# Performance work log

Hardware: AMD Instinct MI355X
Metric: run time of the kernel (lower is better)

## Reference

```python
import jax, jax.numpy as jnp
import numpy as np

D_MODEL = 2048
N_HEADS = 16
HEAD_DIM = D_MODEL // N_HEADS  # 128
MAX_POS = 2048


def _precompute_cos_sin(max_pos, head_dim):
    inv_freq = 1.0 / (10000.0 ** (jnp.arange(0, head_dim, 2, dtype=jnp.float32) / head_dim))
    t = jnp.arange(max_pos, dtype=jnp.float32)
    freqs = jnp.outer(t, inv_freq)          # [max_pos, head_dim//2]
    emb = jnp.concatenate([freqs, freqs], axis=-1)  # [max_pos, head_dim]
    return jnp.cos(emb), jnp.sin(emb)


def _rotate_half(x):
    x1, x2 = x[..., : x.shape[-1] // 2], x[..., x.shape[-1] // 2 :]
    return jnp.concatenate([-x2, x1], axis=-1)


def setup_inputs() -> dict:
    key = jax.random.key(0)
    kx, kq, kk, kv, ko = jax.random.split(key, 5)
    B, S = 2, 2048
    x = jax.random.normal(kx, (B, S, D_MODEL), dtype=jnp.float32)
    scale = 1.0 / np.sqrt(D_MODEL)
    # torch Linear weights are [out_features, in_features]
    Wq = jax.random.normal(kq, (D_MODEL, D_MODEL), dtype=jnp.float32) * scale
    Wk = jax.random.normal(kk, (D_MODEL, D_MODEL), dtype=jnp.float32) * scale
    Wv = jax.random.normal(kv, (D_MODEL, D_MODEL), dtype=jnp.float32) * scale
    Wo = jax.random.normal(ko, (D_MODEL, D_MODEL), dtype=jnp.float32) * scale
    cos, sin = _precompute_cos_sin(MAX_POS, HEAD_DIM)
    # causal mask: True where attention is disallowed (masked_fill semantics)
    mask = jnp.triu(jnp.ones((S, S), dtype=bool), k=1)
    mask = jnp.broadcast_to(mask[None], (B, S, S))
    return {"x": x, "Wq": Wq, "Wk": Wk, "Wv": Wv, "Wo": Wo,
            "cos": cos, "sin": sin, "mask": mask}


def reference(x, Wq, Wk, Wv, Wo, cos, sin, mask):
    B, S, _ = x.shape
    H, Dh = N_HEADS, HEAD_DIM
    scaling = Dh ** -0.5

    def split_heads(y):  # [B,S,D] -> [B,H,S,Dh]
        return y.reshape(B, S, H, Dh).transpose(0, 2, 1, 3)

    q = split_heads(x @ Wq.T)
    k = split_heads(x @ Wk.T)
    v = split_heads(x @ Wv.T)

    c = cos[:S][None, None]  # [1,1,S,Dh]
    s = sin[:S][None, None]
    q = q * c + _rotate_half(q) * s
    k = k * c + _rotate_half(k) * s

    scores = jnp.einsum("bhqd,bhkd->bhqk", q, k) * scaling
    scores = jnp.where(mask[:, None], -jnp.inf, scores)
    attn = jax.nn.softmax(scores, axis=-1)
    out = jnp.einsum("bhqk,bhkd->bhqd", attn, v)  # [B,H,S,Dh]
    out = out.transpose(0, 2, 1, 3).reshape(B, S, H * Dh)
    return out @ Wo.T
```

## Files before the change

kernel.cpp:

```cpp
#include <hip/hip_runtime.h>

typedef float f32x4 __attribute__((ext_vector_type(4)));
typedef short s16x8 __attribute__((ext_vector_type(8)));
typedef unsigned short u16;
typedef u16 u16x4 __attribute__((ext_vector_type(4)));

#define SEQ 2048
#define BATCH 2
#define NH 16
#define DH 128
#define DM 2048
#define MROWS (BATCH * SEQ)

__device__ constexpr float SCALE2 = 0.12751879523531f;

__device__ __forceinline__ u16 f2bf(float f) {
  unsigned u = __float_as_uint(f);
  u += 0x7fffu + ((u >> 16) & 1u);
  return (u16)(u >> 16);
}
__device__ __forceinline__ float bf2f(u16 b) {
  return __uint_as_float(((unsigned)b) << 16);
}

__device__ __forceinline__ void gld_lds16(const void* g, void* l) {
  __builtin_amdgcn_global_load_lds(
      (const __attribute__((address_space(1))) unsigned int*)g,
      (__attribute__((address_space(3))) unsigned int*)l, 16, 0, 0);
}

__global__ __launch_bounds__(256) void cast_all(const float* __restrict__ x,
                                                const float* __restrict__ Wq,
                                                const float* __restrict__ Wk,
                                                const float* __restrict__ Wv,
                                                const float* __restrict__ Wo,
                                                u16* __restrict__ xb,
                                                u16* __restrict__ Wqkvb,
                                                u16* __restrict__ Wob) {
  long i = (long)blockIdx.x * 256 + threadIdx.x;
  const float* src;
  u16* dst;
  long off;
  if (i < 2097152)      { src = x;  dst = xb;              off = i; }
  else if (i < 3145728) { src = Wq; dst = Wqkvb;           off = i - 2097152; }
  else if (i < 4194304) { src = Wk; dst = Wqkvb + 4194304; off = i - 3145728; }
  else if (i < 5242880) { src = Wv; dst = Wqkvb + 8388608; off = i - 4194304; }
  else                  { src = Wo; dst = Wob;             off = i - 5242880; }
  float4 v = ((const float4*)src)[off];
  u16x4 o;
  o[0] = f2bf(v.x); o[1] = f2bf(v.y); o[2] = f2bf(v.z); o[3] = f2bf(v.w);
  ((u16x4*)dst)[off] = o;
}

template <bool F32OUT>
__global__ __launch_bounds__(256) void gemm_bt(const u16* __restrict__ A,
                                               const u16* __restrict__ B,
                                               void* __restrict__ Cv,
                                               int M, int N, int K) {
  __shared__ u16 As[128 * 32];
  __shared__ u16 Bs[128 * 32];
  const int tid = threadIdx.x;
  const int wave = tid >> 6;
  const int lane = tid & 63;
  const int r = lane & 15, g = lane >> 4;

  const int mtiles = M >> 7;
  const int nwg = mtiles * (N >> 7);
  const int cpx = nwg >> 3;
  const int bid = blockIdx.x;
  const int swz = (bid & 7) * cpx + (bid >> 3);
  const int m0 = (swz % mtiles) * 128;
  const int n0 = (swz / mtiles) * 128;

  const int wm = (wave >> 1) * 64;
  const int wn = (wave & 1) * 64;

  f32x4 acc[4][4] = {};

  const int row0 = tid >> 2;
  const int col0 = (tid & 3) * 8;
  const u16* ga0 = A + (long)(m0 + row0) * K + col0;
  const u16* ga1 = A + (long)(m0 + 64 + row0) * K + col0;
  const u16* gb0 = B + (long)(n0 + row0) * K + col0;
  const u16* gb1 = B + (long)(n0 + 64 + row0) * K + col0;

  u16* lA0 = &As[wave * 512];
  u16* lA1 = &As[2048 + wave * 512];
  u16* lB0 = &Bs[wave * 512];
  u16* lB1 = &Bs[2048 + wave * 512];

  for (int k0 = 0; k0 < K; k0 += 32) {
    gld_lds16(ga0 + k0, lA0);
    gld_lds16(ga1 + k0, lA1);
    gld_lds16(gb0 + k0, lB0);
    gld_lds16(gb1 + k0, lB1);
    __syncthreads();
    s16x8 af[4], bfr[4];
#pragma unroll
    for (int i = 0; i < 4; i++) {
      af[i]  = *(const s16x8*)&As[(wm + i * 16 + r) * 32 + g * 8];
      bfr[i] = *(const s16x8*)&Bs[(wn + i * 16 + r) * 32 + g * 8];
    }
#pragma unroll
    for (int i = 0; i < 4; i++)
#pragma unroll
      for (int j = 0; j < 4; j++)
        acc[i][j] = __builtin_amdgcn_mfma_f32_16x16x32_bf16(af[i], bfr[j], acc[i][j], 0, 0, 0);
    __syncthreads();
  }

  float* Cf = (float*)Cv;
  u16* Cb = (u16*)Cv;
#pragma unroll
  for (int i = 0; i < 4; i++)
#pragma unroll
    for (int j = 0; j < 4; j++) {
      const int row = m0 + wm + i * 16 + g * 4;
      const int col = n0 + wn + j * 16 + r;
#pragma unroll
      for (int q = 0; q < 4; q++) {
        float v = acc[i][j][q];
        if (F32OUT) Cf[(long)(row + q) * N + col] = v;
        else        Cb[(long)(row + q) * N + col] = f2bf(v);
      }
    }
}

__global__ __launch_bounds__(512, 2) void gemm_qkv8(const u16* __restrict__ A,
                                                    const u16* __restrict__ B,
                                                    u16* __restrict__ Qo,
                                                    u16* __restrict__ Ko,
                                                    u16* __restrict__ Vo) {
  __shared__ u16 Alds[2][256 * 64];
  __shared__ u16 Blds[2][128 * 64];
  const int tid = threadIdx.x, wave = tid >> 6, lane = tid & 63;
  const int r = lane & 15, g = lane >> 4;
  const int wm = wave >> 1, wn = wave & 1;
  const int bid = blockIdx.x;
  const int swz = (bid & 7) * 96 + (bid >> 3);
  const int m0 = (swz & 15) * 256;
  const int n0 = (swz >> 4) * 128;

  const int lrow = lane >> 3;
  const int csrc = (lane & 7) ^ lrow;

  f32x4 acc[4][4] = {};
  s16x8 aF[2][4], bF[2][4];

#define STAGE_A(TA, MH, BUF) do {                                             \
  _Pragma("unroll") for (int i_ = 0; i_ < 2; ++i_) {                          \
    const int row0_ = (MH) * 128 + i_ * 64 + wave * 8;                        \
    gld_lds16(A + (long)(m0 + row0_ + lrow) * 2048 + (TA) * 64 + csrc * 8,    \
              &Alds[BUF][row0_ * 64]);                                        \
  } } while (0)
#define STAGE_B(TA, NHh, BUF) do {                                            \
    const int row0_ = (NHh) * 64 + wave * 8;                                  \
    gld_lds16(B + (long)(n0 + row0_ + lrow) * 2048 + (TA) * 64 + csrc * 8,    \
              &Blds[BUF][row0_ * 64]);                                        \
  } while (0)

#define READ_K(KK) do {                                                       \
  _Pragma("unroll") for (int mf = 0; mf < 4; ++mf) {                          \
    const int arow = wm * 64 + mf * 16 + r;                                   \
    aF[KK][mf] = *(const s16x8*)&Ab[arow * 64 +                               \
                                    ((((KK) * 4 + g) ^ (arow & 7)) * 8)];     \
  }                                                                           \
  _Pragma("unroll") for (int nf = 0; nf < 4; ++nf) {                          \
    const int brow = wn * 64 + nf * 16 + r;                                   \
    bF[KK][nf] = *(const s16x8*)&Bb[brow * 64 +                               \
                                    ((((KK) * 4 + g) ^ (brow & 7)) * 8)];     \
  } } while (0)

#define MFMA_K(KK) do {                                                       \
  __builtin_amdgcn_s_setprio(1);                                              \
  _Pragma("unroll") for (int mf = 0; mf < 4; ++mf)                            \
    _Pragma("unroll") for (int nf = 0; nf < 4; ++nf)                          \
      acc[mf][nf] = __builtin_amdgcn_mfma_f32_16x16x32_bf16(                  \
          aF[KK][mf], bF[KK][nf], acc[mf][nf], 0, 0, 0);                      \
  __builtin_amdgcn_s_setprio(0);                                              \
} while (0)

  STAGE_A(0, 0, 0); STAGE_B(0, 0, 0); STAGE_A(0, 1, 0); STAGE_B(0, 1, 0);
  STAGE_A(1, 0, 1); STAGE_B(1, 0, 1);
  asm volatile("s_waitcnt vmcnt(3)" ::: "memory");
  __builtin_amdgcn_s_barrier();

  for (int t = 0; t < 32; ++t) {
    const int bt = t & 1, bn = bt ^ 1;
    const u16* Ab = Alds[bt];
    const u16* Bb = Blds[bt];

    READ_K(0);
    __builtin_amdgcn_sched_barrier(0);
    READ_K(1);
    if (t < 31) { STAGE_A(t + 1, 1, bn); STAGE_B(t + 1, 1, bn); }

    asm volatile("s_waitcnt lgkmcnt(8)" ::: "memory");
    __builtin_amdgcn_sched_barrier(0);
    MFMA_K(0);

    asm volatile("s_waitcnt lgkmcnt(0)" ::: "memory");
    __builtin_amdgcn_sched_barrier(0);
    __builtin_amdgcn_s_barrier();

    if (t < 30) { STAGE_A(t + 2, 0, bt); STAGE_B(t + 2, 0, bt); }
    MFMA_K(1);

    if (t < 30)       asm volatile("s_waitcnt vmcnt(3)" ::: "memory");
    else if (t == 30) asm volatile("s_waitcnt vmcnt(0)" ::: "memory");
    __builtin_amdgcn_s_barrier();
  }
#undef MFMA_K
#undef READ_K
#undef STAGE_B
#undef STAGE_A

  u16* Cb = (n0 < 2048) ? Qo : (n0 < 4096 ? Ko : Vo);
  const int nc0 = n0 & 2047;
#pragma unroll
  for (int mi = 0; mi < 4; ++mi)
#pragma unroll
    for (int ni = 0; ni < 4; ++ni)
#pragma unroll
      for (int q = 0; q < 4; ++q)
        Cb[(long)(m0 + wm * 64 + mi * 16 + g * 4 + q) * 2048 +
           nc0 + wn * 64 + ni * 16 + r] = f2bf(acc[mi][ni][q]);
}

__global__ __launch_bounds__(256) void rope_kernel(u16* __restrict__ Q, u16* __restrict__ K,
                                                   const float* __restrict__ cosT,
                                                   const float* __restrict__ sinT) {
  int idx = blockIdx.x * 256 + threadIdx.x;
  int d = idx & 63;
  int h = (idx >> 6) & 15;
  int s = (idx >> 10) & 2047;
  int b = idx >> 21;
  float c = cosT[s * DH + d];
  float sn = sinT[s * DH + d];
  long base = ((long)(b * SEQ + s)) * DM + h * DH + d;
  float q1 = bf2f(Q[base]), q2 = bf2f(Q[base + 64]);
  Q[base]      = f2bf(q1 * c - q2 * sn);
  Q[base + 64] = f2bf(q2 * c + q1 * sn);
  float k1 = bf2f(K[base]), k2 = bf2f(K[base + 64]);
  K[base]      = f2bf(k1 * c - k2 * sn);
  K[base + 64] = f2bf(k2 * c + k1 * sn);
}

__global__ __launch_bounds__(256) void transpose_v(const u16* __restrict__ Vlin,
                                                   u16* __restrict__ Vt) {
  __shared__ u16 tile[64][129];
  int t = threadIdx.x;
  int st = blockIdx.x & 31;
  int h = (blockIdx.x >> 5) & 15;
  int b = blockIdx.x >> 9;
  int s0 = st * 64;
  const u16* src = Vlin + ((long)(b * SEQ + s0)) * DM + h * DH;
#pragma unroll
  for (int rr = 0; rr < 4; rr++) {
    int row = rr * 16 + (t >> 4);
    int col = (t & 15) * 8;
    s16x8 v = *(const s16x8*)&src[(long)row * DM + col];
#pragma unroll
    for (int j = 0; j < 8; j++) tile[row][col + j] = (u16)v[j];
  }
  __syncthreads();
  u16* dst = Vt + ((long)(b * NH + h)) * DH * SEQ + s0;
#pragma unroll
  for (int rr = 0; rr < 4; rr++) {
    int d = rr * 32 + (t >> 3);
    int sc = (t & 7) * 8;
    s16x8 o;
#pragma unroll
    for (int j = 0; j < 8; j++) o[j] = (short)tile[sc + j][d];
    *(s16x8*)&dst[(long)d * SEQ + sc] = o;
  }
}


__device__ __forceinline__ void softmax_swapped(
    f32x4 (&s)[4], float& mi, float& li,
    u16 (&pl)[16][64], float (&als)[16],
    int qbase, int k0, int r, int g) {
  const int q = qbase + r;
  const bool edge = (k0 + 63) > qbase;
  float v[16];
#pragma unroll
  for (int kk = 0; kk < 4; kk++)
#pragma unroll
    for (int i = 0; i < 4; i++) {
      float x = s[kk][i] * SCALE2;
      if (edge && (k0 + kk * 16 + g * 4 + i > q)) x = -1e30f;
      v[kk * 4 + i] = x;
    }
  float t8[8], t4[4];
#pragma unroll
  for (int j = 0; j < 8; j++) t8[j] = fmaxf(v[2 * j], v[2 * j + 1]);
#pragma unroll
  for (int j = 0; j < 4; j++) t4[j] = fmaxf(t8[2 * j], t8[2 * j + 1]);
  float mx = fmaxf(fmaxf(t4[0], t4[1]), fmaxf(t4[2], t4[3]));
  mx = fmaxf(mx, __shfl_xor(mx, 16, 64));
  mx = fmaxf(mx, __shfl_xor(mx, 32, 64));
  const float mnew = fmaxf(mi, mx);
  const float a = exp2f(mi - mnew);
  float p[16];
#pragma unroll
  for (int j = 0; j < 16; j++) p[j] = exp2f(v[j] - mnew);
  float s8[8], s4[4];
#pragma unroll
  for (int j = 0; j < 8; j++) s8[j] = p[2 * j] + p[2 * j + 1];
#pragma unroll
  for (int j = 0; j < 4; j++) s4[j] = s8[2 * j] + s8[2 * j + 1];
  float ps = (s4[0] + s4[1]) + (s4[2] + s4[3]);
  ps += __shfl_xor(ps, 16, 64);
  ps += __shfl_xor(ps, 32, 64);
  li = li * a + ps;
  mi = mnew;
  const int sw = (r & 7) << 3;
#pragma unroll
  for (int kk = 0; kk < 4; kk++) {
    u16x4 w;
#pragma unroll
    for (int i = 0; i < 4; i++) w[i] = f2bf(p[kk * 4 + i]);
    *(u16x4*)&pl[r][(kk * 16 + g * 4) ^ sw] = w;
  }
  als[r] = a;
}

__global__ __launch_bounds__(512, 4) void attn_kernel(const u16* __restrict__ Q,
                                                      const u16* __restrict__ K,
                                                      const u16* __restrict__ Vt,
                                                      u16* __restrict__ O) {
  __shared__ u16 Klds[64 * 128];
  __shared__ u16 Vlds[128 * 64];
  __shared__ u16 Plds[8][16][64];
  __shared__ float Alds[8][16];

  const int tid = threadIdx.x, wave = tid >> 6, lane = tid & 63;
  const int r = lane & 15, g = lane >> 4;
  const int bh = blockIdx.x & 31;
  const int j = blockIdx.x >> 5;
  const int h = bh & 15, b = bh >> 4;
  const bool isB = wave >= 4;
  const int w4 = wave & 3;
  const int strip = isB ? (31 - j) : j;
  const int q0 = strip * 64 + w4 * 16;
  const int nt = 32 - j;
  const int lastA = j;

  const u16* Qbh = Q + (long)b * SEQ * DM + h * DH;
  const u16* Kbh = K + (long)b * SEQ * DM + h * DH;
  const u16* Vbh = Vt + ((long)(b * NH + h)) * DH * SEQ;

  s16x8 qf[4];
#pragma unroll
  for (int jj = 0; jj < 4; jj++)
    qf[jj] = *(const s16x8*)&Qbh[(long)(q0 + r) * DM + jj * 32 + g * 8];

  f32x4 oacc[8] = {};
  float mi = -1e30f, li = 0.f;

  for (int kt = 0; kt < nt; ++kt) {
    const int k0 = kt * 64;
    __syncthreads();
#pragma unroll
    for (int c = 0; c < 2; ++c) {
      const int s = c * 512 + tid;
      const int krow = s >> 4;
      const int kch = (s & 15) ^ (krow & 7);
      gld_lds16(Kbh + (long)(k0 + krow) * DM + kch * 8,
                &Klds[(c * 512 + wave * 64) * 8]);
      const int vrow = s >> 3;
      const int vch = (s & 7) ^ (vrow & 7);
      gld_lds16(Vbh + (long)vrow * SEQ + k0 + vch * 8,
                &Vlds[(c * 512 + wave * 64) * 8]);
    }
    __syncthreads();

    const bool active = isB || (kt <= lastA);
    if (active) {
      f32x4 sacc[4] = {};
#pragma unroll
      for (int kk = 0; kk < 4; kk++) {
#pragma unroll
        for (int jj = 0; jj < 4; jj++) {
          s16x8 kf = *(const s16x8*)&Klds[(kk * 16 + r) * 128 +
                                          (((jj * 4 + g) ^ (r & 7)) * 8)];
          sacc[kk] = __builtin_amdgcn_mfma_f32_16x16x32_bf16(kf, qf[jj], sacc[kk], 0, 0, 0);
        }
      }
      softmax_swapped(sacc, mi, li, Plds[wave], Alds[wave], q0, k0, r, g);

      f32x4 av = *(const f32x4*)&Alds[wave][g * 4];
#pragma unroll
      for (int f = 0; f < 8; f++)
#pragma unroll
        for (int i = 0; i < 4; i++) oacc[f][i] *= av[i];

      const int sw = (r & 7) << 3;
#pragma unroll
      for (int kc = 0; kc < 2; kc++) {
        s16x8 pf = *(const s16x8*)&Plds[wave][r][(kc * 32 + g * 8) ^ sw];
#pragma unroll
        for (int f = 0; f < 8; f++) {
          s16x8 vf = *(const s16x8*)&Vlds[(f * 16 + r) * 64 +
                                          (((kc * 4 + g) ^ (r & 7)) * 8)];
          oacc[f] = __builtin_amdgcn_mfma_f32_16x16x32_bf16(pf, vf, oacc[f], 0, 0, 0);
        }
      }
    }
  }

  Alds[wave][r] = 1.f / li;
  f32x4 iv = *(const f32x4*)&Alds[wave][g * 4];
  u16* Obh = O + (long)b * SEQ * DM + h * DH;
#pragma unroll
  for (int f = 0; f < 8; f++)
#pragma unroll
    for (int i = 0; i < 4; i++)
      Obh[(long)(q0 + g * 4 + i) * DM + f * 16 + r] = f2bf(oacc[f][i] * iv[i]);
}

extern "C" void kernel_launch(void* const* d_in, const int* in_sizes, int n_in,
                              void* d_out, int out_size, void* d_ws, size_t ws_size,
                              hipStream_t stream) {
  const float* x    = (const float*)d_in[0];
  const float* Wq   = (const float*)d_in[1];
  const float* Wk   = (const float*)d_in[2];
  const float* Wv   = (const float*)d_in[3];
  const float* Wo   = (const float*)d_in[4];
  const float* cosT = (const float*)d_in[5];
  const float* sinT = (const float*)d_in[6];

  if (ws_size < (size_t)134217728) return;

  char* ws = (char*)d_ws;
  u16* xb    = (u16*)(ws);
  u16* Wqkvb = (u16*)(ws + 16777216);
  u16* Wob   = (u16*)(ws + 41943040);
  u16* Qlin  = (u16*)(ws + 50331648);
  u16* Klin  = (u16*)(ws + 67108864);
  u16* Vlin  = (u16*)(ws + 83886080);
  u16* Vt    = (u16*)(ws + 100663296);
  u16* Olin  = (u16*)(ws + 117440512);

  cast_all<<<24576, 256, 0, stream>>>(x, Wq, Wk, Wv, Wo, xb, Wqkvb, Wob);

  gemm_qkv8<<<768, 512, 0, stream>>>(xb, Wqkvb, Qlin, Klin, Vlin);

  rope_kernel<<<16384, 256, 0, stream>>>(Qlin, Klin, cosT, sinT);
  transpose_v<<<1024, 256, 0, stream>>>(Vlin, Vt);
  attn_kernel<<<512, 512, 0, stream>>>(Qlin, Klin, Vt, Olin);

  gemm_bt<true><<<512, 256, 0, stream>>>(Olin, Wob, d_out, MROWS, DM, DM);
}
```

Before: 284.1 us.

## Split tail key tiles across idle waves and merge partial softmax states

```diff
diff --git a/kernel.cpp b/kernel.cpp
--- a/kernel.cpp
+++ b/kernel.cpp
@@ -277,51 +277,55 @@
 }
 
 
-__device__ __forceinline__ void softmax_swapped(
-    f32x4 (&s)[4], float& mi, float& li,
+template <int NKK>
+__device__ __forceinline__ void softmax_sw(
+    f32x4 (&s)[NKK], float& mi, float& li,
     u16 (&pl)[16][64], float (&als)[16],
-    int qbase, int k0, int r, int g) {
+    int qbase, int k0, int kkbase, int r, int g) {
   const int q = qbase + r;
-  const bool edge = (k0 + 63) > qbase;
-  float v[16];
-#pragma unroll
-  for (int kk = 0; kk < 4; kk++)
+  const bool edge = (k0 + (kkbase + NKK) * 16 - 1) > qbase;
+  float v[NKK * 4];
+#pragma unroll
+  for (int kk = 0; kk < NKK; kk++)
 #pragma unroll
     for (int i = 0; i < 4; i++) {
       float x = s[kk][i] * SCALE2;
-      if (edge && (k0 + kk * 16 + g * 4 + i > q)) x = -1e30f;
+      if (edge && (k0 + (kkbase + kk) * 16 + g * 4 + i > q)) x = -1e30f;
       v[kk * 4 + i] = x;
     }
-  float t8[8], t4[4];
-#pragma unroll
-  for (int j = 0; j < 8; j++) t8[j] = fmaxf(v[2 * j], v[2 * j + 1]);
-#pragma unroll
-  for (int j = 0; j < 4; j++) t4[j] = fmaxf(t8[2 * j], t8[2 * j + 1]);
-  float mx = fmaxf(fmaxf(t4[0], t4[1]), fmaxf(t4[2], t4[3]));
+  float t[NKK * 4];
+#pragma unroll
+  for (int i = 0; i < NKK * 4; i++) t[i] = v[i];
+#pragma unroll
+  for (int w = NKK * 2; w >= 1; w >>= 1)
+#pragma unroll
+    for (int i = 0; i < w; i++) t[i] = fmaxf(t[i], t[i + w]);
+  float mx = t[0];
   mx = fmaxf(mx, __shfl_xor(mx, 16, 64));
   mx = fmaxf(mx, __shfl_xor(mx, 32, 64));
   const float mnew = fmaxf(mi, mx);
   const float a = exp2f(mi - mnew);
-  float p[16];
-#pragma unroll
-  for (int j = 0; j < 16; j++) p[j] = exp2f(v[j] - mnew);
-  float s8[8], s4[4];
-#pragma unroll
-  for (int j = 0; j < 8; j++) s8[j] = p[2 * j] + p[2 * j + 1];
-#pragma unroll
-  for (int j = 0; j < 4; j++) s4[j] = s8[2 * j] + s8[2 * j + 1];
-  float ps = (s4[0] + s4[1]) + (s4[2] + s4[3]);
+  float p[NKK * 4];
+#pragma unroll
+  for (int i = 0; i < NKK * 4; i++) p[i] = exp2f(v[i] - mnew);
+#pragma unroll
+  for (int i = 0; i < NKK * 4; i++) t[i] = p[i];
+#pragma unroll
+  for (int w = NKK * 2; w >= 1; w >>= 1)
+#pragma unroll
+    for (int i = 0; i < w; i++) t[i] += t[i + w];
+  float ps = t[0];
   ps += __shfl_xor(ps, 16, 64);
   ps += __shfl_xor(ps, 32, 64);
   li = li * a + ps;
   mi = mnew;
   const int sw = (r & 7) << 3;
 #pragma unroll
-  for (int kk = 0; kk < 4; kk++) {
+  for (int kk = 0; kk < NKK; kk++) {
     u16x4 w;
 #pragma unroll
     for (int i = 0; i < 4; i++) w[i] = f2bf(p[kk * 4 + i]);
-    *(u16x4*)&pl[r][(kk * 16 + g * 4) ^ sw] = w;
+    *(u16x4*)&pl[r][((kkbase + kk) * 16 + g * 4) ^ sw] = w;
   }
   als[r] = a;
 }
@@ -330,27 +334,30 @@
                                                       const u16* __restrict__ K,
                                                       const u16* __restrict__ Vt,
                                                       u16* __restrict__ O) {
-  __shared__ u16 Klds[64 * 128];
-  __shared__ u16 Vlds[128 * 64];
+  __shared__ __align__(16) u16 Klds[64 * 128];
+  __shared__ __align__(16) u16 Vlds[128 * 64];
   __shared__ u16 Plds[8][16][64];
   __shared__ float Alds[8][16];
+  __shared__ float MLx[4][64][2];
 
   const int tid = threadIdx.x, wave = tid >> 6, lane = tid & 63;
   const int r = lane & 15, g = lane >> 4;
   const int bh = blockIdx.x & 31;
-  const int j = blockIdx.x >> 5;
+  const int jp = blockIdx.x >> 5;
   const int h = bh & 15, b = bh >> 4;
   const bool isB = wave >= 4;
   const int w4 = wave & 3;
-  const int strip = isB ? (31 - j) : j;
-  const int q0 = strip * 64 + w4 * 16;
-  const int nt = 32 - j;
-  const int lastA = j;
+  const int h2 = wave >> 2;
+  const int q0A = jp * 64 + w4 * 16;
+  const int q0B = (31 - jp) * 64 + w4 * 16;
+  const int nt = 32 - jp;
 
   const u16* Qbh = Q + (long)b * SEQ * DM + h * DH;
   const u16* Kbh = K + (long)b * SEQ * DM + h * DH;
   const u16* Vbh = Vt + ((long)(b * NH + h)) * DH * SEQ;
-
+  u16* Obh = O + (long)b * SEQ * DM + h * DH;
+
+  int q0 = isB ? q0B : q0A;
   s16x8 qf[4];
 #pragma unroll
   for (int jj = 0; jj < 4; jj++)
@@ -376,27 +383,23 @@
     }
     __syncthreads();
 
-    const bool active = isB || (kt <= lastA);
-    if (active) {
+    const int sw = (r & 7) << 3;
+    if (kt <= jp) {
       f32x4 sacc[4] = {};
 #pragma unroll
-      for (int kk = 0; kk < 4; kk++) {
+      for (int kk = 0; kk < 4; kk++)
 #pragma unroll
         for (int jj = 0; jj < 4; jj++) {
           s16x8 kf = *(const s16x8*)&Klds[(kk * 16 + r) * 128 +
                                           (((jj * 4 + g) ^ (r & 7)) * 8)];
           sacc[kk] = __builtin_amdgcn_mfma_f32_16x16x32_bf16(kf, qf[jj], sacc[kk], 0, 0, 0);
         }
-      }
-      softmax_swapped(sacc, mi, li, Plds[wave], Alds[wave], q0, k0, r, g);
-
+      softmax_sw<4>(sacc, mi, li, Plds[wave], Alds[wave], q0, k0, 0, r, g);
       f32x4 av = *(const f32x4*)&Alds[wave][g * 4];
 #pragma unroll
       for (int f = 0; f < 8; f++)
 #pragma unroll
         for (int i = 0; i < 4; i++) oacc[f][i] *= av[i];
-
-      const int sw = (r & 7) << 3;
 #pragma unroll
       for (int kc = 0; kc < 2; kc++) {
         s16x8 pf = *(const s16x8*)&Plds[wave][r][(kc * 32 + g * 8) ^ sw];
@@ -407,17 +410,83 @@
           oacc[f] = __builtin_amdgcn_mfma_f32_16x16x32_bf16(pf, vf, oacc[f], 0, 0, 0);
         }
       }
+      if (kt == jp && !isB) {
+        Alds[wave][r] = 1.f / li;
+        f32x4 iv = *(const f32x4*)&Alds[wave][g * 4];
+#pragma unroll
+        for (int f = 0; f < 8; f++)
+#pragma unroll
+          for (int i = 0; i < 4; i++)
+            Obh[(long)(q0 + g * 4 + i) * DM + f * 16 + r] = f2bf(oacc[f][i] * iv[i]);
+        q0 = q0B;
+#pragma unroll
+        for (int jj = 0; jj < 4; jj++)
+          qf[jj] = *(const s16x8*)&Qbh[(long)(q0 + r) * DM + jj * 32 + g * 8];
+        mi = -1e30f; li = 0.f;
+#pragma unroll
+        for (int f = 0; f < 8; f++) oacc[f] = (f32x4){0.f, 0.f, 0.f, 0.f};
+      }
+    } else {
+      f32x4 sacc[2] = {};
+#pragma unroll
+      for (int kkl = 0; kkl < 2; kkl++)
+#pragma unroll
+        for (int jj = 0; jj < 4; jj++) {
+          s16x8 kf = *(const s16x8*)&Klds[((h2 * 2 + kkl) * 16 + r) * 128 +
+                                          (((jj * 4 + g) ^ (r & 7)) * 8)];
+          sacc[kkl] = __builtin_amdgcn_mfma_f32_16x16x32_bf16(kf, qf[jj], sacc[kkl], 0, 0, 0);
+        }
+      softmax_sw<2>(sacc, mi, li, Plds[wave], Alds[wave], q0, k0, h2 * 2, r, g);
+      f32x4 av = *(const f32x4*)&Alds[wave][g * 4];
+#pragma unroll
+      for (int f = 0; f < 8; f++)
+#pragma unroll
+        for (int i = 0; i < 4; i++) oacc[f][i] *= av[i];
+      s16x8 pf = *(const s16x8*)&Plds[wave][r][(h2 * 32 + g * 8) ^ sw];
+#pragma unroll
+      for (int f = 0; f < 8; f++) {
+        s16x8 vf = *(const s16x8*)&Vlds[(f * 16 + r) * 64 +
+                                        (((h2 * 4 + g) ^ (r & 7)) * 8)];
+        oacc[f] = __builtin_amdgcn_mfma_f32_16x16x32_bf16(pf, vf, oacc[f], 0, 0, 0);
+      }
     }
   }
 
-  Alds[wave][r] = 1.f / li;
-  f32x4 iv = *(const f32x4*)&Alds[wave][g * 4];
-  u16* Obh = O + (long)b * SEQ * DM + h * DH;
-#pragma unroll
-  for (int f = 0; f < 8; f++)
-#pragma unroll
-    for (int i = 0; i < 4; i++)
-      Obh[(long)(q0 + g * 4 + i) * DM + f * 16 + r] = f2bf(oacc[f][i] * iv[i]);
+  __syncthreads();
+  float* xbuf = (w4 < 2) ? ((float*)Klds + w4 * 2048) : ((float*)Vlds + (w4 - 2) * 2048);
+  if (!isB) {
+    float* dst = xbuf + lane * 32;
+#pragma unroll
+    for (int f = 0; f < 8; f++) *(f32x4*)(dst + f * 4) = oacc[f];
+    MLx[w4][lane][0] = mi;
+    MLx[w4][lane][1] = li;
+  }
+  __syncthreads();
+  if (isB) {
+    const float* src = xbuf + lane * 32;
+    const float m2 = MLx[w4][lane][0];
+    const float l2 = MLx[w4][lane][1];
+    const float m = fmaxf(mi, m2);
+    const float a1 = exp2f(mi - m);
+    const float a2 = exp2f(m2 - m);
+    const float inv = 1.f / (li * a1 + l2 * a2);
+    Alds[wave][r]     = a1 * inv;
+    Alds[wave - 4][r] = a2 * inv;
+    f32x4 w1 = *(const f32x4*)&Alds[wave][g * 4];
+    f32x4 w2 = *(const f32x4*)&Alds[wave - 4][g * 4];
+#pragma unroll
+    for (int f = 0; f < 8; f++) {
+      f32x4 o2 = *(const f32x4*)(src + f * 4);
+#pragma unroll
+      for (int i = 0; i < 4; i++)
+        oacc[f][i] = oacc[f][i] * w1[i] + o2[i] * w2[i];
+    }
+#pragma unroll
+    for (int f = 0; f < 8; f++)
+#pragma unroll
+      for (int i = 0; i < 4; i++)
+        Obh[(long)(q0 + g * 4 + i) * DM + f * 16 + r] = f2bf(oacc[f][i]);
+  }
 }
 
 extern "C" void kernel_launch(void* const* d_in, const int* in_sizes, int n_in,
```

Measured after the change: 344.9 us. 1.21x slower.

## Use pipelined 256x128 GEMM for output projection and reorder attention block scheduling

Applied to the files above, without the earlier changes.

```diff
diff --git a/kernel.cpp b/kernel.cpp
--- a/kernel.cpp
+++ b/kernel.cpp
@@ -52,100 +52,45 @@
   ((u16x4*)dst)[off] = o;
 }
 
-template <bool F32OUT>
-__global__ __launch_bounds__(256) void gemm_bt(const u16* __restrict__ A,
-                                               const u16* __restrict__ B,
-                                               void* __restrict__ Cv,
-                                               int M, int N, int K) {
-  __shared__ u16 As[128 * 32];
-  __shared__ u16 Bs[128 * 32];
-  const int tid = threadIdx.x;
-  const int wave = tid >> 6;
-  const int lane = tid & 63;
-  const int r = lane & 15, g = lane >> 4;
-
-  const int mtiles = M >> 7;
-  const int nwg = mtiles * (N >> 7);
-  const int cpx = nwg >> 3;
-  const int bid = blockIdx.x;
-  const int swz = (bid & 7) * cpx + (bid >> 3);
-  const int m0 = (swz % mtiles) * 128;
-  const int n0 = (swz / mtiles) * 128;
-
-  const int wm = (wave >> 1) * 64;
-  const int wn = (wave & 1) * 64;
-
-  f32x4 acc[4][4] = {};
-
-  const int row0 = tid >> 2;
-  const int col0 = (tid & 3) * 8;
-  const u16* ga0 = A + (long)(m0 + row0) * K + col0;
-  const u16* ga1 = A + (long)(m0 + 64 + row0) * K + col0;
-  const u16* gb0 = B + (long)(n0 + row0) * K + col0;
-  const u16* gb1 = B + (long)(n0 + 64 + row0) * K + col0;
-
-  u16* lA0 = &As[wave * 512];
-  u16* lA1 = &As[2048 + wave * 512];
-  u16* lB0 = &Bs[wave * 512];
-  u16* lB1 = &Bs[2048 + wave * 512];
-
-  for (int k0 = 0; k0 < K; k0 += 32) {
-    gld_lds16(ga0 + k0, lA0);
-    gld_lds16(ga1 + k0, lA1);
-    gld_lds16(gb0 + k0, lB0);
-    gld_lds16(gb1 + k0, lB1);
-    __syncthreads();
-    s16x8 af[4], bfr[4];
-#pragma unroll
-    for (int i = 0; i < 4; i++) {
-      af[i]  = *(const s16x8*)&As[(wm + i * 16 + r) * 32 + g * 8];
-      bfr[i] = *(const s16x8*)&Bs[(wn + i * 16 + r) * 32 + g * 8];
-    }
-#pragma unroll
-    for (int i = 0; i < 4; i++)
-#pragma unroll
-      for (int j = 0; j < 4; j++)
-        acc[i][j] = __builtin_amdgcn_mfma_f32_16x16x32_bf16(af[i], bfr[j], acc[i][j], 0, 0, 0);
-    __syncthreads();
-  }
-
-  float* Cf = (float*)Cv;
-  u16* Cb = (u16*)Cv;
-#pragma unroll
-  for (int i = 0; i < 4; i++)
-#pragma unroll
-    for (int j = 0; j < 4; j++) {
-      const int row = m0 + wm + i * 16 + g * 4;
-      const int col = n0 + wn + j * 16 + r;
-#pragma unroll
-      for (int q = 0; q < 4; q++) {
-        float v = acc[i][j][q];
-        if (F32OUT) Cf[(long)(row + q) * N + col] = v;
-        else        Cb[(long)(row + q) * N + col] = f2bf(v);
-      }
-    }
-}
-
-__global__ __launch_bounds__(512, 2) void gemm_qkv8(const u16* __restrict__ A,
-                                                    const u16* __restrict__ B,
-                                                    u16* __restrict__ Qo,
-                                                    u16* __restrict__ Ko,
-                                                    u16* __restrict__ Vo) {
-  __shared__ u16 Alds[2][256 * 64];
-  __shared__ u16 Blds[2][128 * 64];
-  const int tid = threadIdx.x, wave = tid >> 6, lane = tid & 63;
-  const int r = lane & 15, g = lane >> 4;
-  const int wm = wave >> 1, wn = wave & 1;
-  const int bid = blockIdx.x;
-  const int swz = (bid & 7) * 96 + (bid >> 3);
-  const int m0 = (swz & 15) * 256;
-  const int n0 = (swz >> 4) * 128;
-
-  const int lrow = lane >> 3;
-  const int csrc = (lane & 7) ^ lrow;
-
-  f32x4 acc[4][4] = {};
-  s16x8 aF[2][4], bF[2][4];
+
+#define GEMM_V3_BODY(A, B, NTILE_SHIFT)                                       \
+  __shared__ u16 Alds[2][256 * 64];                                           \
+  __shared__ u16 Blds[2][128 * 64];                                           \
+  const int tid = threadIdx.x, wave = tid >> 6, lane = tid & 63;              \
+  const int r = lane & 15, g = lane >> 4;                                     \
+  const int wm = wave >> 1, wn = wave & 1;                                    \
+  const int bid = blockIdx.x;                                                 \
+  const int swz = (bid & 7) * (gridDim.x >> 3) + (bid >> 3);                  \
+  const int m0 = (swz & 15) * 256;                                            \
+  const int n0 = (swz >> 4) * 128;                                            \
+  const int lrow = lane >> 3;                                                 \
+  const int csrc = (lane & 7) ^ lrow;                                         \
+  f32x4 acc[4][4] = {};                                                       \
+  s16x8 aF[2][4], bF[2][4];                                                   \
+  STAGE_A(0, 0, 0); STAGE_B(0, 0, 0); STAGE_A(0, 1, 0); STAGE_B(0, 1, 0);     \
+  STAGE_A(1, 0, 1); STAGE_B(1, 0, 1);                                         \
+  asm volatile("s_waitcnt vmcnt(3)" ::: "memory");                            \
+  __builtin_amdgcn_s_barrier();                                               \
+  for (int t = 0; t < 32; ++t) {                                              \
+    const int bt = t & 1, bn = bt ^ 1;                                        \
+    const u16* Ab = Alds[bt];                                                 \
+    const u16* Bb = Blds[bt];                                                 \
+    READ_K(0);                                                                \
+    __builtin_amdgcn_sched_barrier(0);                                        \
+    READ_K(1);                                                                \
+    if (t < 31) { STAGE_A(t + 1, 1, bn); STAGE_B(t + 1, 1, bn); }             \
+    asm volatile("s_waitcnt lgkmcnt(8)" ::: "memory");                        \
+    __builtin_amdgcn_sched_barrier(0);                                        \
+    MFMA_K(0);                                                                \
+    asm volatile("s_waitcnt lgkmcnt(0)" ::: "memory");                        \
+    __builtin_amdgcn_sched_barrier(0);                                        \
+    __builtin_amdgcn_s_barrier();                                             \
+    if (t < 30) { STAGE_A(t + 2, 0, bt); STAGE_B(t + 2, 0, bt); }             \
+    MFMA_K(1);                                                                \
+    if (t < 30)       asm volatile("s_waitcnt vmcnt(3)" ::: "memory");        \
+    else if (t == 30) asm volatile("s_waitcnt vmcnt(0)" ::: "memory");        \
+    __builtin_amdgcn_s_barrier();                                             \
+  }
 
 #define STAGE_A(TA, MH, BUF) do {                                             \
   _Pragma("unroll") for (int i_ = 0; i_ < 2; ++i_) {                          \
@@ -158,7 +103,6 @@
     gld_lds16(B + (long)(n0 + row0_ + lrow) * 2048 + (TA) * 64 + csrc * 8,    \
               &Blds[BUF][row0_ * 64]);                                        \
   } while (0)
-
 #define READ_K(KK) do {                                                       \
   _Pragma("unroll") for (int mf = 0; mf < 4; ++mf) {                          \
     const int arow = wm * 64 + mf * 16 + r;                                   \
@@ -170,7 +114,6 @@
     bF[KK][nf] = *(const s16x8*)&Bb[brow * 64 +                               \
                                     ((((KK) * 4 + g) ^ (brow & 7)) * 8)];     \
   } } while (0)
-
 #define MFMA_K(KK) do {                                                       \
   __builtin_amdgcn_s_setprio(1);                                              \
   _Pragma("unroll") for (int mf = 0; mf < 4; ++mf)                            \
@@ -180,52 +123,43 @@
   __builtin_amdgcn_s_setprio(0);                                              \
 } while (0)
 
-  STAGE_A(0, 0, 0); STAGE_B(0, 0, 0); STAGE_A(0, 1, 0); STAGE_B(0, 1, 0);
-  STAGE_A(1, 0, 1); STAGE_B(1, 0, 1);
-  asm volatile("s_waitcnt vmcnt(3)" ::: "memory");
-  __builtin_amdgcn_s_barrier();
-
-  for (int t = 0; t < 32; ++t) {
-    const int bt = t & 1, bn = bt ^ 1;
-    const u16* Ab = Alds[bt];
-    const u16* Bb = Blds[bt];
-
-    READ_K(0);
-    __builtin_amdgcn_sched_barrier(0);
-    READ_K(1);
-    if (t < 31) { STAGE_A(t + 1, 1, bn); STAGE_B(t + 1, 1, bn); }
-
-    asm volatile("s_waitcnt lgkmcnt(8)" ::: "memory");
-    __builtin_amdgcn_sched_barrier(0);
-    MFMA_K(0);
-
-    asm volatile("s_waitcnt lgkmcnt(0)" ::: "memory");
-    __builtin_amdgcn_sched_barrier(0);
-    __builtin_amdgcn_s_barrier();
-
-    if (t < 30) { STAGE_A(t + 2, 0, bt); STAGE_B(t + 2, 0, bt); }
-    MFMA_K(1);
-
-    if (t < 30)       asm volatile("s_waitcnt vmcnt(3)" ::: "memory");
-    else if (t == 30) asm volatile("s_waitcnt vmcnt(0)" ::: "memory");
-    __builtin_amdgcn_s_barrier();
-  }
+__global__ __launch_bounds__(512, 2) void gemm_qkv8(const u16* __restrict__ A,
+                                                    const u16* __restrict__ B,
+                                                    u16* __restrict__ Qo,
+                                                    u16* __restrict__ Ko,
+                                                    u16* __restrict__ Vo) {
+  GEMM_V3_BODY(A, B, 4)
+  u16* Cb = (n0 < 2048) ? Qo : (n0 < 4096 ? Ko : Vo);
+  const int nc0 = n0 & 2047;
+#pragma unroll
+  for (int mi = 0; mi < 4; ++mi)
+#pragma unroll
+    for (int ni = 0; ni < 4; ++ni)
+#pragma unroll
+      for (int q = 0; q < 4; ++q)
+        Cb[(long)(m0 + wm * 64 + mi * 16 + g * 4 + q) * 2048 +
+           nc0 + wn * 64 + ni * 16 + r] = f2bf(acc[mi][ni][q]);
+}
+
+__global__ __launch_bounds__(512, 2) void gemm_wo(const u16* __restrict__ A,
+                                                  const u16* __restrict__ B,
+                                                  float* __restrict__ C) {
+  GEMM_V3_BODY(A, B, 4)
+#pragma unroll
+  for (int mi = 0; mi < 4; ++mi)
+#pragma unroll
+    for (int ni = 0; ni < 4; ++ni)
+#pragma unroll
+      for (int q = 0; q < 4; ++q)
+        C[(long)(m0 + wm * 64 + mi * 16 + g * 4 + q) * 2048 +
+          n0 + wn * 64 + ni * 16 + r] = acc[mi][ni][q];
+}
+
 #undef MFMA_K
 #undef READ_K
 #undef STAGE_B
 #undef STAGE_A
-
-  u16* Cb = (n0 < 2048) ? Qo : (n0 < 4096 ? Ko : Vo);
-  const int nc0 = n0 & 2047;
-#pragma unroll
-  for (int mi = 0; mi < 4; ++mi)
-#pragma unroll
-    for (int ni = 0; ni < 4; ++ni)
-#pragma unroll
-      for (int q = 0; q < 4; ++q)
-        Cb[(long)(m0 + wm * 64 + mi * 16 + g * 4 + q) * 2048 +
-           nc0 + wn * 64 + ni * 16 + r] = f2bf(acc[mi][ni][q]);
-}
+#undef GEMM_V3_BODY
 
 __global__ __launch_bounds__(256) void rope_kernel(u16* __restrict__ Q, u16* __restrict__ K,
                                                    const float* __restrict__ cosT,
@@ -338,7 +272,8 @@
   const int tid = threadIdx.x, wave = tid >> 6, lane = tid & 63;
   const int r = lane & 15, g = lane >> 4;
   const int bh = blockIdx.x & 31;
-  const int j = blockIdx.x >> 5;
+  const int jj = blockIdx.x >> 5;
+  const int j = (jj < 8) ? jj : 23 - jj;
   const int h = bh & 15, b = bh >> 4;
   const bool isB = wave >= 4;
   const int w4 = wave & 3;
@@ -353,8 +288,8 @@
 
   s16x8 qf[4];
 #pragma unroll
-  for (int jj = 0; jj < 4; jj++)
-    qf[jj] = *(const s16x8*)&Qbh[(long)(q0 + r) * DM + jj * 32 + g * 8];
+  for (int jq = 0; jq < 4; jq++)
+    qf[jq] = *(const s16x8*)&Qbh[(long)(q0 + r) * DM + jq * 32 + g * 8];
 
   f32x4 oacc[8] = {};
   float mi = -1e30f, li = 0.f;
@@ -382,10 +317,10 @@
 #pragma unroll
       for (int kk = 0; kk < 4; kk++) {
 #pragma unroll
-        for (int jj = 0; jj < 4; jj++) {
+        for (int jq = 0; jq < 4; jq++) {
           s16x8 kf = *(const s16x8*)&Klds[(kk * 16 + r) * 128 +
-                                          (((jj * 4 + g) ^ (r & 7)) * 8)];
-          sacc[kk] = __builtin_amdgcn_mfma_f32_16x16x32_bf16(kf, qf[jj], sacc[kk], 0, 0, 0);
+                                          (((jq * 4 + g) ^ (r & 7)) * 8)];
+          sacc[kk] = __builtin_amdgcn_mfma_f32_16x16x32_bf16(kf, qf[jq], sacc[kk], 0, 0, 0);
         }
       }
       softmax_swapped(sacc, mi, li, Plds[wave], Alds[wave], q0, k0, r, g);
@@ -451,5 +386,5 @@
   transpose_v<<<1024, 256, 0, stream>>>(Vlin, Vt);
   attn_kernel<<<512, 512, 0, stream>>>(Qlin, Klin, Vt, Olin);
 
-  gemm_bt<true><<<512, 256, 0, stream>>>(Olin, Wob, d_out, MROWS, DM, DM);
-}
+  gemm_wo<<<256, 512, 0, stream>>>(Olin, Wob, (float*)d_out);
+}
```

Result: faster. 264.9 us (-6.8%).
